# Kernel optimization log

Measured on AMD Instinct MI355X. Metric: run time of the kernel, lower is better.

Reference implementation:

```python
import jax, jax.numpy as jnp
import numpy as np

LN_EPS = 1e-12
B, L, D, V, PATCH, IMG, C = 64, 40, 768, 30522, 16, 384, 3
GRID = IMG // PATCH            # 24
NPATCH = GRID * GRID           # 576


def layer_norm(x, g, b):
    m = jnp.mean(x, axis=-1, keepdims=True)
    v = jnp.var(x, axis=-1, keepdims=True)
    return (x - m) * jax.lax.rsqrt(v + LN_EPS) * g + b


def setup_inputs() -> dict:
    key = jax.random.key(0)
    ks = jax.random.split(key, 12)
    s = 0.02
    return {
        "input_ids": jax.random.randint(ks[0], (B, L), 0, V, dtype=jnp.int32),
        "attention_mask": jnp.ones((B, L), jnp.int32),
        "token_type_ids": jnp.zeros((B, L), jnp.int32),
        "pixel_values": jax.random.normal(ks[1], (B, C, IMG, IMG), jnp.float32),
        "pixel_mask": jnp.ones((B, IMG, IMG), jnp.int32),
        "word_emb": jax.random.normal(ks[2], (V, D), jnp.float32) * s,
        "text_pos_emb": jax.random.normal(ks[3], (L, D), jnp.float32) * s,
        "text_tok_emb": jax.random.normal(ks[4], (2, D), jnp.float32) * s,
        "ln_g": jnp.ones((D,), jnp.float32),
        "ln_b": jnp.zeros((D,), jnp.float32),
        "conv_w": jax.random.normal(ks[5], (D, C, PATCH, PATCH), jnp.float32) * s,
        "conv_b": jnp.zeros((D,), jnp.float32),
        "cls_token": jnp.zeros((1, 1, D), jnp.float32),
        "vis_pos_emb": jax.random.normal(ks[6], (1, NPATCH + 1, D), jnp.float32) * s,
        "mod_type_emb": jax.random.normal(ks[7], (2, D), jnp.float32) * s,
    }


def reference(input_ids, attention_mask, token_type_ids, pixel_values, pixel_mask,
              word_emb, text_pos_emb, text_tok_emb, ln_g, ln_b,
              conv_w, conv_b, cls_token, vis_pos_emb, mod_type_emb):
    # ---- text embeddings (BERT-style) ----
    te = word_emb[input_ids] + text_pos_emb[None, :, :] + text_tok_emb[token_type_ids]
    te = layer_norm(te, ln_g, ln_b)  # [B, L, D]

    # ---- visual_embed ----
    # patch projection conv (stride = patch size)
    x = jax.lax.conv_general_dilated(
        pixel_values, conv_w, window_strides=(PATCH, PATCH), padding='VALID',
        dimension_numbers=('NCHW', 'OIHW', 'NCHW')) + conv_b[None, :, None, None]
    # [B, D, 24, 24] -> [B, 576, D]
    x = x.reshape(B, D, NPATCH).transpose(0, 2, 1)
    # full pixel_mask => x_h = x_w = GRID for every sample; bilinear interp of the
    # [1, D, 24, 24] spatial pos-embed to (24, 24) with align_corners=True is identity,
    # all patches valid, valid_nums == max_image_length => selection is identity.
    pos_embed = vis_pos_emb[:, 1:, :]           # [1, NPATCH, D]
    img = x + pos_embed                          # [B, NPATCH, D]
    image_masks = jnp.ones((B, NPATCH), attention_mask.dtype)

    # ---- modality type embeddings ----
    te = te + mod_type_emb[0][None, None, :]
    img = img + mod_type_emb[1][None, None, :]

    # ---- concat with cls token ----
    emb = jnp.concatenate([te, img], axis=1)
    cls = jnp.broadcast_to(cls_token, (B, 1, D))
    emb = jnp.concatenate([cls, emb], axis=1)    # [B, 1+L+NPATCH, D]
    masks = jnp.concatenate(
        [jnp.ones((B, 1), attention_mask.dtype), attention_mask, image_masks], axis=1)
    return emb, masks
```

## Files before the change

kernel.cpp:

```cpp
#include <hip/hip_runtime.h>

typedef __attribute__((ext_vector_type(4))) float f4;
typedef __attribute__((ext_vector_type(4))) float f32x4;
typedef __attribute__((ext_vector_type(8))) __bf16 bf8;
typedef __attribute__((ext_vector_type(8))) unsigned short us8;

#define NB 64
#define LSEQ 40
#define D_DIM 768
#define NPATCH 576
#define SEQ 617
#define K_DIM 768
#define M_DIM (NB * NPATCH)
#define GEMM_LDS 131072

static __device__ __forceinline__ unsigned short f2bf(float f) {
    union { float f; unsigned u; } v; v.f = f;
    unsigned r = v.u + 0x7FFFu + ((v.u >> 16) & 1u);
    return (unsigned short)(r >> 16);
}

static __device__ __forceinline__ void gload_lds16(const void* g, void* l) {
    __builtin_amdgcn_global_load_lds(
        (const __attribute__((address_space(1))) unsigned int*)g,
        (__attribute__((address_space(3))) unsigned int*)l,
        16, 0, 0);
}

#define MFMA16(a, b, c) __builtin_amdgcn_mfma_f32_16x16x32_bf16((a), (b), (c), 0, 0, 0)

__global__ __launch_bounds__(256) void prep_w(const float* __restrict__ cw,
                                              unsigned short* __restrict__ wo) {
    int t = blockIdx.x * 256 + threadIdx.x;
    int cs = t % 96, n = t / 96;
    int blk8 = cs >> 3, c = cs & 7;
    int cl = (blk8 << 3) | (c ^ (n & 7));
    const float* s = cw + (size_t)n * 768 + cl * 8;
    f4 a = *(const f4*)s;
    f4 b = *(const f4*)(s + 4);
    us8 r;
    r[0]=f2bf(a[0]); r[1]=f2bf(a[1]); r[2]=f2bf(a[2]); r[3]=f2bf(a[3]);
    r[4]=f2bf(b[0]); r[5]=f2bf(b[1]); r[6]=f2bf(b[2]); r[7]=f2bf(b[3]);
    *(us8*)(wo + (size_t)n * 768 + cs * 8) = r;
}

__global__ __launch_bounds__(512, 2) void gemm_patch(
    const float* __restrict__ px, const __bf16* __restrict__ W,
    const float* __restrict__ conv_b, const float* __restrict__ vis_pos,
    const float* __restrict__ mod, float* __restrict__ out,
    const int* __restrict__ ids, const int* __restrict__ tti,
    const float* __restrict__ we, const float* __restrict__ pe,
    const float* __restrict__ tke, const float* __restrict__ lng,
    const float* __restrict__ lnb, const float* __restrict__ cls,
    const int* __restrict__ am) {
    extern __shared__ __align__(16) char smem[];
    char* Ab0 = smem;
    char* Ab1 = smem + 32768;
    char* Bb0 = smem + 65536;
    char* Bb1 = smem + 98304;

    const int tid = threadIdx.x;
    const int w = tid >> 6, lane = tid & 63;

    int lid = blockIdx.x;
    int gwi = (lid & 7) * 54 + (lid >> 3);
    const int tile_n = (gwi % 3) * 256;
    const int tile_m = (gwi / 3) * 256;
    const int wm = w >> 2, wn = w & 3;
    const int wr = wm * 128, wc = wn * 64;

    f32x4 acc[8][4] = {};
    const char* Bb = (const char*)W;
    const int rsel = lane & 15;
    const int hk = lane >> 4;

    const int arow = tid & 255;
    const int ii0 = tid >> 8;
    int agm = tile_m + arow;
    int abimg = agm / 576, ap = agm % 576;
    int aph = ap / 24, apw = ap % 24;
    const float* pxrow = px + (size_t)abimg * 442368
                            + (size_t)(aph * 16) * 384 + apw * 16;

    f4 areg[2][4];
    auto LOAD_A = [&](int kt) {
        int c = kt >> 2, i0 = (kt & 3) << 2;
#pragma unroll
        for (int rep = 0; rep < 2; ++rep) {
            int i = i0 + ii0 + rep * 2;
            const float* s = pxrow + (size_t)c * 147456 + i * 384;
#pragma unroll
            for (int q = 0; q < 4; ++q) areg[rep][q] = *(const f4*)(s + q * 4);
        }
    };
    auto WRITE_A = [&](char* dst) {
#pragma unroll
        for (int rep = 0; rep < 2; ++rep) {
            int ii = ii0 + rep * 2;
            us8 h0, h1;
#pragma unroll
            for (int q = 0; q < 2; ++q) {
                h0[q*4+0]=f2bf(areg[rep][q][0]); h0[q*4+1]=f2bf(areg[rep][q][1]);
                h0[q*4+2]=f2bf(areg[rep][q][2]); h0[q*4+3]=f2bf(areg[rep][q][3]);
                h1[q*4+0]=f2bf(areg[rep][q+2][0]); h1[q*4+1]=f2bf(areg[rep][q+2][1]);
                h1[q*4+2]=f2bf(areg[rep][q+2][2]); h1[q*4+3]=f2bf(areg[rep][q+2][3]);
            }
            int cc0 = ii * 2;
            *(us8*)(dst + arow * 128 + ((cc0    ) ^ (arow & 7)) * 16) = h0;
            *(us8*)(dst + arow * 128 + ((cc0 + 1) ^ (arow & 7)) * 16) = h1;
        }
    };
    auto STAGE_B = [&](char* lbase, int kt) {
#pragma unroll
        for (int i = 0; i < 4; ++i) {
            int uoff = (w << 10) + i * 8192;
            int loff = uoff + (lane << 4);
            int row = loff >> 7, col = loff & 127;
            gload_lds16(Bb + (size_t)(tile_n + row) * 1536 + kt * 128 + col,
                        lbase + uoff);
        }
    };

    LOAD_A(0);
    STAGE_B(Bb0, 0);
    WRITE_A(Ab0);
    __syncthreads();

    for (int t = 0; t < 12; ++t) {
        char* Ac = (t & 1) ? Ab1 : Ab0;
        char* Bc = (t & 1) ? Bb1 : Bb0;
        char* An = (t & 1) ? Ab0 : Ab1;
        char* Bn = (t & 1) ? Bb0 : Bb1;

        if (t < 11) {
            LOAD_A(t + 1);
            STAGE_B(Bn, t + 1);
        }

        bf8 a0[4][2], b0[4][2];
#pragma unroll
        for (int mi = 0; mi < 4; ++mi) {
            int r = wr + mi * 16 + rsel;
#pragma unroll
            for (int ks = 0; ks < 2; ++ks) {
                int cst = (ks * 4 + hk) ^ (r & 7);
                a0[mi][ks] = *(const bf8*)(Ac + r * 128 + cst * 16);
            }
        }
#pragma unroll
        for (int ni = 0; ni < 4; ++ni) {
            int r = wc + ni * 16 + rsel;
#pragma unroll
            for (int ks = 0; ks < 2; ++ks) {
                int cst = (ks * 4 + hk) ^ (r & 7);
                b0[ni][ks] = *(const bf8*)(Bc + r * 128 + cst * 16);
            }
        }
#pragma unroll
        for (int mi = 0; mi < 4; ++mi)
#pragma unroll
            for (int ni = 0; ni < 4; ++ni) {
                acc[mi][ni] = MFMA16(a0[mi][0], b0[ni][0], acc[mi][ni]);
                acc[mi][ni] = MFMA16(a0[mi][1], b0[ni][1], acc[mi][ni]);
            }

        bf8 a1[4][2];
#pragma unroll
        for (int mi = 0; mi < 4; ++mi) {
            int r = wr + 64 + mi * 16 + rsel;
#pragma unroll
            for (int ks = 0; ks < 2; ++ks) {
                int cst = (ks * 4 + hk) ^ (r & 7);
                a1[mi][ks] = *(const bf8*)(Ac + r * 128 + cst * 16);
            }
        }
#pragma unroll
        for (int mi = 0; mi < 4; ++mi)
#pragma unroll
            for (int ni = 0; ni < 4; ++ni) {
                acc[4 + mi][ni] = MFMA16(a1[mi][0], b0[ni][0], acc[4 + mi][ni]);
                acc[4 + mi][ni] = MFMA16(a1[mi][1], b0[ni][1], acc[4 + mi][ni]);
            }

        if (t < 11) {
            WRITE_A(An);
            __syncthreads();
        }
    }

    {
        const int lr = (lane >> 4) * 4;
        const int lc = lane & 15;
        int gnv[4]; float cv[4];
#pragma unroll
        for (int ni = 0; ni < 4; ++ni) {
            gnv[ni] = tile_n + wc + ni * 16 + lc;
            cv[ni] = conv_b[gnv[ni]] + mod[768 + gnv[ni]];
        }
#pragma unroll
        for (int mi = 0; mi < 8; ++mi) {
            int gm0 = tile_m + wr + mi * 16 + lr;
            int bimg0 = gm0 / 576;
            int pp0 = gm0 - bimg0 * 576;
#pragma unroll
            for (int r = 0; r < 4; ++r) {
                int bimg = bimg0, pp2 = pp0 + r;
                if (pp2 >= 576) { bimg++; pp2 -= 576; }
                const float* vp = vis_pos + (size_t)(pp2 + 1) * 768;
                float* op = out + ((size_t)bimg * SEQ + 1 + LSEQ + pp2) * 768;
#pragma unroll
                for (int ni = 0; ni < 4; ++ni)
                    op[gnv[ni]] = acc[mi][ni][r] + cv[ni] + vp[gnv[ni]];
            }
        }
    }

    {
        int row = blockIdx.x * 8 + w;
        if (row < 2560) {
            int b = row / 40, l = row % 40;
            const float* wp = we + (size_t)ids[row] * 768;
            const float* pp = pe + l * 768;
            const float* tp = tke + (size_t)tti[row] * 768;
            f4 x[3];
            float s = 0.f, q = 0.f;
#pragma unroll
            for (int j = 0; j < 3; ++j) {
                int d = j * 256 + lane * 4;
                f4 v = *(const f4*)(wp + d);
                f4 v2 = *(const f4*)(pp + d);
                f4 v3 = *(const f4*)(tp + d);
                v = v + v2 + v3;
                x[j] = v;
                s += v[0] + v[1] + v[2] + v[3];
                q += v[0]*v[0] + v[1]*v[1] + v[2]*v[2] + v[3]*v[3];
            }
#pragma unroll
            for (int o = 32; o > 0; o >>= 1) { s += __shfl_xor(s, o); q += __shfl_xor(q, o); }
            float mean = s * (1.0f / 768.0f);
            float var = q * (1.0f / 768.0f) - mean * mean;
            float rstd = rsqrtf(var + 1e-12f);
            float* op = out + ((size_t)b * SEQ + 1 + l) * 768;
#pragma unroll
            for (int j = 0; j < 3; ++j) {
                int d = j * 256 + lane * 4;
                f4 gg = *(const f4*)(lng + d);
                f4 bv = *(const f4*)(lnb + d);
                f4 mm = *(const f4*)(mod + d);
                f4 r = (x[j] - mean) * rstd * gg + bv + mm;
                *(f4*)(op + d) = r;
            }
        }
    }

    {
        int t2 = blockIdx.x * 512 + tid;
        if (t2 < NB * 768) {
            int b = t2 / 768, d = t2 % 768;
            out[(size_t)b * SEQ * 768 + d] = cls[d];
        } else if (t2 < NB * 768 + NB * SEQ) {
            int i = t2 - NB * 768;
            int b = i / SEQ, s = i % SEQ;
            float v = 1.0f;
            if (s >= 1 && s <= LSEQ) v = (float)am[b * LSEQ + s - 1];
            out[(size_t)NB * SEQ * 768 + i] = v;
        }
    }
}

extern "C" void kernel_launch(void* const* d_in, const int* in_sizes, int n_in,
                              void* d_out, int out_size, void* d_ws, size_t ws_size,
                              hipStream_t stream) {
    const int*   ids  = (const int*)d_in[0];
    const int*   am   = (const int*)d_in[1];
    const int*   tti  = (const int*)d_in[2];
    const float* px   = (const float*)d_in[3];
    const float* we   = (const float*)d_in[5];
    const float* pe   = (const float*)d_in[6];
    const float* tke  = (const float*)d_in[7];
    const float* lng  = (const float*)d_in[8];
    const float* lnb  = (const float*)d_in[9];
    const float* cw   = (const float*)d_in[10];
    const float* cb   = (const float*)d_in[11];
    const float* cls  = (const float*)d_in[12];
    const float* vpos = (const float*)d_in[13];
    const float* mod  = (const float*)d_in[14];
    float* out = (float*)d_out;

    __bf16* Wbf = (__bf16*)d_ws;

    hipFuncSetAttribute((const void*)gemm_patch,
                        hipFuncAttributeMaxDynamicSharedMemorySize, GEMM_LDS);

    prep_w<<<288, 256, 0, stream>>>(cw, (unsigned short*)Wbf);
    gemm_patch<<<432, 512, GEMM_LDS, stream>>>(px, Wbf, cb, vpos, mod, out,
                                               ids, tti, we, pe, tke, lng, lnb,
                                               cls, am);
}
```

Measured before the change: 99.63 us.

## Halve the patch GEMM M-tile to 128 rows and double the grid

The patch-projection GEMM now uses 128x256 tiles instead of 256x256. Each wave keeps one 64x64 accumulator block rather than two, and each thread loads a single A row segment per k-step. Shared memory for the A buffers shrinks, cutting per-block LDS to 96KB, and the grid grows to 864 blocks. The aim is better load balance across CUs and lower per-block register and LDS pressure. The cost is less reuse of each staged B tile and more total B traffic and synchronisation.

```diff
diff --git a/kernel.cpp b/kernel.cpp
--- a/kernel.cpp
+++ b/kernel.cpp
@@ -12,7 +12,7 @@
 #define SEQ 617
 #define K_DIM 768
 #define M_DIM (NB * NPATCH)
-#define GEMM_LDS 131072
+#define GEMM_LDS 98304
 
 static __device__ __forceinline__ unsigned short f2bf(float f) {
     union { float f; unsigned u; } v; v.f = f;
@@ -55,60 +55,52 @@
     const int* __restrict__ am) {
     extern __shared__ __align__(16) char smem[];
     char* Ab0 = smem;
-    char* Ab1 = smem + 32768;
-    char* Bb0 = smem + 65536;
-    char* Bb1 = smem + 98304;
+    char* Ab1 = smem + 16384;
+    char* Bb0 = smem + 32768;
+    char* Bb1 = smem + 65536;
 
     const int tid = threadIdx.x;
     const int w = tid >> 6, lane = tid & 63;
 
     int lid = blockIdx.x;
-    int gwi = (lid & 7) * 54 + (lid >> 3);
+    int gwi = (lid & 7) * 108 + (lid >> 3);
     const int tile_n = (gwi % 3) * 256;
-    const int tile_m = (gwi / 3) * 256;
-    const int wm = w >> 2, wn = w & 3;
-    const int wr = wm * 128, wc = wn * 64;
-
-    f32x4 acc[8][4] = {};
+    const int tile_m = (gwi / 3) * 128;
+    const int wr = (w >> 2) * 64;
+    const int wc = (w & 3) * 64;
+
+    f32x4 acc[4][4] = {};
     const char* Bb = (const char*)W;
     const int rsel = lane & 15;
     const int hk = lane >> 4;
 
-    const int arow = tid & 255;
-    const int ii0 = tid >> 8;
+    const int arow = tid >> 2;
+    const int q4 = tid & 3;
     int agm = tile_m + arow;
     int abimg = agm / 576, ap = agm % 576;
     int aph = ap / 24, apw = ap % 24;
     const float* pxrow = px + (size_t)abimg * 442368
                             + (size_t)(aph * 16) * 384 + apw * 16;
 
-    f4 areg[2][4];
+    f4 areg[4];
     auto LOAD_A = [&](int kt) {
         int c = kt >> 2, i0 = (kt & 3) << 2;
-#pragma unroll
-        for (int rep = 0; rep < 2; ++rep) {
-            int i = i0 + ii0 + rep * 2;
-            const float* s = pxrow + (size_t)c * 147456 + i * 384;
-#pragma unroll
-            for (int q = 0; q < 4; ++q) areg[rep][q] = *(const f4*)(s + q * 4);
-        }
+        const float* s = pxrow + (size_t)c * 147456 + (i0 + q4) * 384;
+#pragma unroll
+        for (int q = 0; q < 4; ++q) areg[q] = *(const f4*)(s + q * 4);
     };
     auto WRITE_A = [&](char* dst) {
-#pragma unroll
-        for (int rep = 0; rep < 2; ++rep) {
-            int ii = ii0 + rep * 2;
-            us8 h0, h1;
-#pragma unroll
-            for (int q = 0; q < 2; ++q) {
-                h0[q*4+0]=f2bf(areg[rep][q][0]); h0[q*4+1]=f2bf(areg[rep][q][1]);
-                h0[q*4+2]=f2bf(areg[rep][q][2]); h0[q*4+3]=f2bf(areg[rep][q][3]);
-                h1[q*4+0]=f2bf(areg[rep][q+2][0]); h1[q*4+1]=f2bf(areg[rep][q+2][1]);
-                h1[q*4+2]=f2bf(areg[rep][q+2][2]); h1[q*4+3]=f2bf(areg[rep][q+2][3]);
-            }
-            int cc0 = ii * 2;
-            *(us8*)(dst + arow * 128 + ((cc0    ) ^ (arow & 7)) * 16) = h0;
-            *(us8*)(dst + arow * 128 + ((cc0 + 1) ^ (arow & 7)) * 16) = h1;
-        }
+        us8 h0, h1;
+#pragma unroll
+        for (int q = 0; q < 2; ++q) {
+            h0[q*4+0]=f2bf(areg[q][0]);   h0[q*4+1]=f2bf(areg[q][1]);
+            h0[q*4+2]=f2bf(areg[q][2]);   h0[q*4+3]=f2bf(areg[q][3]);
+            h1[q*4+0]=f2bf(areg[q+2][0]); h1[q*4+1]=f2bf(areg[q+2][1]);
+            h1[q*4+2]=f2bf(areg[q+2][2]); h1[q*4+3]=f2bf(areg[q+2][3]);
+        }
+        int cc0 = q4 * 2;
+        *(us8*)(dst + arow * 128 + ((cc0    ) ^ (arow & 7)) * 16) = h0;
+        *(us8*)(dst + arow * 128 + ((cc0 + 1) ^ (arow & 7)) * 16) = h1;
     };
     auto STAGE_B = [&](char* lbase, int kt) {
 #pragma unroll
@@ -164,24 +156,6 @@
                 acc[mi][ni] = MFMA16(a0[mi][1], b0[ni][1], acc[mi][ni]);
             }
 
-        bf8 a1[4][2];
-#pragma unroll
-        for (int mi = 0; mi < 4; ++mi) {
-            int r = wr + 64 + mi * 16 + rsel;
-#pragma unroll
-            for (int ks = 0; ks < 2; ++ks) {
-                int cst = (ks * 4 + hk) ^ (r & 7);
-                a1[mi][ks] = *(const bf8*)(Ac + r * 128 + cst * 16);
-            }
-        }
-#pragma unroll
-        for (int mi = 0; mi < 4; ++mi)
-#pragma unroll
-            for (int ni = 0; ni < 4; ++ni) {
-                acc[4 + mi][ni] = MFMA16(a1[mi][0], b0[ni][0], acc[4 + mi][ni]);
-                acc[4 + mi][ni] = MFMA16(a1[mi][1], b0[ni][1], acc[4 + mi][ni]);
-            }
-
         if (t < 11) {
             WRITE_A(An);
             __syncthreads();
@@ -198,7 +172,7 @@
             cv[ni] = conv_b[gnv[ni]] + mod[768 + gnv[ni]];
         }
 #pragma unroll
-        for (int mi = 0; mi < 8; ++mi) {
+        for (int mi = 0; mi < 4; ++mi) {
             int gm0 = tile_m + wr + mi * 16 + lr;
             int bimg0 = gm0 / 576;
             int pp0 = gm0 - bimg0 * 576;
@@ -293,7 +267,7 @@
                         hipFuncAttributeMaxDynamicSharedMemorySize, GEMM_LDS);
 
     prep_w<<<288, 256, 0, stream>>>(cw, (unsigned short*)Wbf);
-    gemm_patch<<<432, 512, GEMM_LDS, stream>>>(px, Wbf, cb, vpos, mod, out,
+    gemm_patch<<<864, 512, GEMM_LDS, stream>>>(px, Wbf, cb, vpos, mod, out,
                                                ids, tti, we, pe, tke, lng, lnb,
                                                cls, am);
 }
```

Result: slower. 124.4 us (+24.8%).
